# Optimization experiments

Hardware: AMD Instinct MI355X
Metric: run time of the kernel (lower is better)

The kernel has to match this reference:

```python
import jax, jax.numpy as jnp
import numpy as np


def setup_inputs() -> dict:
    key = jax.random.key(0)
    k1, k2, k3 = jax.random.split(key, 3)
    N1, N2, P, D = 4, 8, 1024, 128  # P = PH*PW = 32*32 (512px / 16 patch)
    feats = jax.random.normal(k1, (N1, P, D), dtype=jnp.float32)
    nfeats = jax.random.normal(k2, (N2, P, D), dtype=jnp.float32)
    background_masks = jax.random.uniform(k3, (N1, P), dtype=jnp.float32)
    return {"feats": feats, "nfeats": nfeats, "background_masks": background_masks,
            "PH": 32, "PW": 32, "H": 512, "W": 512}


def reference(feats, nfeats, background_masks, PH, PW, H, W):
    # L2-normalize patch embeddings (as in `f / f.norm(dim=-1, keepdim=True)`)
    f = feats / jnp.linalg.norm(feats, axis=-1, keepdims=True)    # [N1,P,D]
    g = nfeats / jnp.linalg.norm(nfeats, axis=-1, keepdims=True)  # [N2,Q,D]
    # Euclidean cdist of unit vectors: d^2 = 2 - 2*dot (clamped at 0)
    dot = jnp.einsum('npd,mqd->nmpq', f, g)                        # [N1,N2,P,Q]
    dist = jnp.sqrt(jnp.maximum(2.0 - 2.0 * dot, 0.0)) / 2.0      # cdist/2, permuted
    # min over normal patches Q -> per-query-patch nearest-neighbor distance
    scores_patch = dist.min(axis=-1)                               # [N1,N2,P]
    scores_patch = scores_patch * background_masks[:, None, :]
    # image score: max over query patches, mean over normal images
    scores = scores_patch.max(axis=-1).mean(axis=-1)               # [N1]
    # pixel map: mean over normal images, reshape to patch grid, bilinear upsample
    sp = scores_patch.mean(axis=1).reshape(-1, PH, PW)             # [N1,PH,PW]
    scores_pixel = jax.image.resize(sp, (sp.shape[0], H, W), method='bilinear')
    return scores, scores_pixel
```

## Files before the change

### kernel.cpp

```cpp
#include <hip/hip_runtime.h>

typedef __attribute__((ext_vector_type(8))) short short8;
typedef __attribute__((ext_vector_type(4))) float f32x4;
typedef __attribute__((ext_vector_type(4))) unsigned int u32x4;

static __device__ inline unsigned short f2bf(float x) {
    unsigned int u = __float_as_uint(x);
    u = (u + 0x7FFFu + ((u >> 16) & 1u)) >> 16;
    return (unsigned short)u;
}

__global__ __launch_bounds__(256) void knorm(const float* __restrict__ feats,
                                             const float* __restrict__ nfeats,
                                             unsigned short* __restrict__ fb,
                                             unsigned short* __restrict__ gb) {
    int row = blockIdx.x * 4 + (threadIdx.x >> 6);
    int lane = threadIdx.x & 63;
    const float* src;
    unsigned short* dst;
    if (row < 4096) { src = feats + row * 128;           dst = fb + row * 128; }
    else            { src = nfeats + (row - 4096) * 128; dst = gb + (row - 4096) * 128; }
    float2 v = ((const float2*)src)[lane];
    float ss = v.x * v.x + v.y * v.y;
    #pragma unroll
    for (int d = 32; d; d >>= 1) ss += __shfl_xor(ss, d);
    float inv = 1.0f / sqrtf(ss);
    ushort2 o;
    o.x = f2bf(v.x * inv);
    o.y = f2bf(v.y * inv);
    ((ushort2*)dst)[lane] = o;
}

__global__ __launch_bounds__(512, 2) void kscore(const unsigned short* __restrict__ fb,
                                                 const unsigned short* __restrict__ gb,
                                                 float* __restrict__ sp_part) {
    __shared__ char gtile[2][8192];
    const int tid = threadIdx.x;
    const int lane = tid & 63;
    const int wave = tid >> 6;
    const int wp = wave >> 1, wqt = wave & 1;
    const int l15 = lane & 15, lhi = lane >> 4;
    const int m = blockIdx.x;
    const int ptile = blockIdx.y >> 1, qh = blockIdx.y & 1;
    const int rowbase = ptile * 256 + wp * 64;

    const unsigned short* gBase = gb + ((size_t)m * 1024 + qh * 512) * 128;

    const int sr = tid >> 4, sc = tid & 15;
    const unsigned short* gsrc = gBase + (size_t)sr * 128 + sc * 8;
    const int wofs = (sr * 256 + sc * 16) ^ ((sr & 7) << 4);

    short8 a[4][4];
    #pragma unroll
    for (int pg = 0; pg < 4; pg++) {
        const unsigned short* arow = fb + (size_t)(rowbase + pg * 16 + l15) * 128;
        #pragma unroll
        for (int kk = 0; kk < 4; kk++)
            a[pg][kk] = *(const short8*)(arow + kk * 32 + lhi * 8);
    }

    f32x4 mx[4];
    #pragma unroll
    for (int pg = 0; pg < 4; pg++)
        #pragma unroll
        for (int i = 0; i < 4; i++) mx[pg][i] = -1e30f;

    u32x4 st0 = *(const u32x4*)(gsrc);
    *(u32x4*)(gtile[0] + wofs) = st0;
    u32x4 stn = *(const u32x4*)(gsrc + 32 * 128);
    asm volatile("s_waitcnt lgkmcnt(0)" ::: "memory");
    __builtin_amdgcn_s_barrier();

    #pragma unroll
    for (int t = 0; t < 16; t++) {
        __builtin_amdgcn_sched_barrier(0);
        u32x4 stnn;
        if (t < 14) stnn = *(const u32x4*)(gsrc + (size_t)(t + 2) * 32 * 128);
        if (t < 15) *(u32x4*)(gtile[(t + 1) & 1] + wofs) = stn;
        const char* tp = gtile[t & 1];
        const int r = wqt * 16 + l15;
        const int rowoff = r * 256;
        const int swz = (r & 7) << 4;
        f32x4 acc[4];
        #pragma unroll
        for (int pg = 0; pg < 4; pg++)
            #pragma unroll
            for (int i = 0; i < 4; i++) acc[pg][i] = 0.f;
        #pragma unroll
        for (int kk = 0; kk < 4; kk++) {
            short8 b = *(const short8*)(tp + ((rowoff + kk * 64 + lhi * 16) ^ swz));
            #pragma unroll
            for (int pg = 0; pg < 4; pg++)
                acc[pg] = __builtin_amdgcn_mfma_f32_16x16x32_bf16(a[pg][kk], b, acc[pg], 0, 0, 0);
        }
        #pragma unroll
        for (int pg = 0; pg < 4; pg++)
            #pragma unroll
            for (int i = 0; i < 4; i++) mx[pg][i] = fmaxf(mx[pg][i], acc[pg][i]);
        if (t < 14) stn = stnn;
        asm volatile("s_waitcnt lgkmcnt(0)" ::: "memory");
        __builtin_amdgcn_s_barrier();
    }

    #pragma unroll
    for (int pg = 0; pg < 4; pg++)
        #pragma unroll
        for (int i = 0; i < 4; i++) {
            float v = mx[pg][i];
            v = fmaxf(v, __shfl_xor(v, 1));
            v = fmaxf(v, __shfl_xor(v, 2));
            v = fmaxf(v, __shfl_xor(v, 4));
            v = fmaxf(v, __shfl_xor(v, 8));
            mx[pg][i] = v;
        }
    if (l15 == 0) {
        const int slot = qh * 2 + wqt;
        #pragma unroll
        for (int pg = 0; pg < 4; pg++)
            #pragma unroll
            for (int i = 0; i < 4; i++) {
                int row = rowbase + pg * 16 + lhi * 4 + i;
                int n = row >> 10, p = row & 1023;
                sp_part[((size_t)(n * 8 + m) * 4 + slot) * 1024 + p] = mx[pg][i];
            }
    }
}

__global__ __launch_bounds__(256) void kfinal(const float* __restrict__ sp_part,
                                              const float* __restrict__ mask,
                                              float* __restrict__ out) {
    const int n = blockIdx.y;
    const int bx = blockIdx.x;
    const int t = threadIdx.x;
    float* pix = out + 4;

    if (bx == 64) {
        __shared__ float smax[4];
        float acc = 0.f;
        for (int m = 0; m < 8; m++) {
            const float* base = sp_part + (size_t)(n * 8 + m) * 4 * 1024;
            float lm = -1e30f;
            #pragma unroll
            for (int i = 0; i < 4; i++) {
                int p = i * 256 + t;
                float dot = fmaxf(fmaxf(base[p], base[1024 + p]),
                                  fmaxf(base[2048 + p], base[3072 + p]));
                float d = sqrtf(fmaxf(2.0f - 2.0f * dot, 0.0f)) * 0.5f * mask[n * 1024 + p];
                lm = fmaxf(lm, d);
            }
            #pragma unroll
            for (int d = 32; d; d >>= 1) lm = fmaxf(lm, __shfl_xor(lm, d));
            if ((t & 63) == 0) smax[t >> 6] = lm;
            __syncthreads();
            if (t == 0) acc += fmaxf(fmaxf(smax[0], smax[1]), fmaxf(smax[2], smax[3]));
            __syncthreads();
        }
        if (t == 0) out[n] = acc * 0.125f;
        return;
    }

    __shared__ float sp_row[2][32];
    const int band = bx * 8;
    const int pr_lo = (int)floorf((band + 0.5f) * 0.0625f - 0.5f);
    const int row0 = min(max(pr_lo, 0), 31);
    const int row1 = min(max(pr_lo + 1, 0), 31);
    {
        int v = t >> 2, sub = t & 3;
        int vr = v >> 5, vc = v & 31;
        int p = (vr ? row1 : row0) * 32 + vc;
        float sum = 0.f;
        #pragma unroll
        for (int mi = 0; mi < 2; mi++) {
            int m = sub * 2 + mi;
            const float* base = sp_part + (size_t)(n * 8 + m) * 4 * 1024 + p;
            float dot = fmaxf(fmaxf(base[0], base[1024]),
                              fmaxf(base[2048], base[3072]));
            sum += sqrtf(fmaxf(2.0f - 2.0f * dot, 0.0f)) * 0.5f;
        }
        sum *= mask[n * 1024 + p];
        sum += __shfl_xor(sum, 1);
        sum += __shfl_xor(sum, 2);
        if (sub == 0) sp_row[vr][vc] = sum * 0.125f;
    }
    __syncthreads();
    #pragma unroll
    for (int i = 0; i < 16; i++) {
        int idx = i * 256 + t;
        int yl = idx >> 9, x = idx & 511;
        int y = band + yl;
        float fy = (y + 0.5f) * 0.0625f - 0.5f;
        float ty = fy - (float)pr_lo;
        float fx = (x + 0.5f) * 0.0625f - 0.5f;
        float xf = floorf(fx);
        float tx = fx - xf;
        int x0 = (int)xf;
        int x0c = min(max(x0, 0), 31), x1c = min(max(x0 + 1, 0), 31);
        float v00 = sp_row[0][x0c], v01 = sp_row[0][x1c];
        float v10 = sp_row[1][x0c], v11 = sp_row[1][x1c];
        float v0 = v00 + tx * (v01 - v00);
        float v1 = v10 + tx * (v11 - v10);
        pix[(size_t)n * 262144 + (size_t)y * 512 + x] = v0 + ty * (v1 - v0);
    }
}

extern "C" void kernel_launch(void* const* d_in, const int* in_sizes, int n_in,
                              void* d_out, int out_size, void* d_ws, size_t ws_size,
                              hipStream_t stream) {
    const float* feats = (const float*)d_in[0];
    const float* nfeats = (const float*)d_in[1];
    const float* mask = (const float*)d_in[2];
    float* out = (float*)d_out;

    unsigned short* fb = (unsigned short*)d_ws;
    unsigned short* gb = fb + 4096 * 128;
    float* sp_part = (float*)((char*)d_ws + 3u * 1024u * 1024u);

    knorm<<<3072, 256, 0, stream>>>(feats, nfeats, fb, gb);
    kscore<<<dim3(8, 32), 512, 0, stream>>>(fb, gb, sp_part);
    kfinal<<<dim3(65, 4), 256, 0, stream>>>(sp_part, mask, out);
}
```

Baseline: 31.05 us.

## Split kscore into 256-thread blocks covering quarter Q ranges, each wave doing both q-tiles

```diff
diff --git a/kernel.cpp b/kernel.cpp
--- a/kernel.cpp
+++ b/kernel.cpp
@@ -31,24 +31,26 @@
     ((ushort2*)dst)[lane] = o;
 }
 
-__global__ __launch_bounds__(512, 2) void kscore(const unsigned short* __restrict__ fb,
+__global__ __launch_bounds__(256, 2) void kscore(const unsigned short* __restrict__ fb,
                                                  const unsigned short* __restrict__ gb,
                                                  float* __restrict__ sp_part) {
     __shared__ char gtile[2][8192];
     const int tid = threadIdx.x;
     const int lane = tid & 63;
     const int wave = tid >> 6;
-    const int wp = wave >> 1, wqt = wave & 1;
     const int l15 = lane & 15, lhi = lane >> 4;
     const int m = blockIdx.x;
-    const int ptile = blockIdx.y >> 1, qh = blockIdx.y & 1;
-    const int rowbase = ptile * 256 + wp * 64;
-
-    const unsigned short* gBase = gb + ((size_t)m * 1024 + qh * 512) * 128;
-
-    const int sr = tid >> 4, sc = tid & 15;
-    const unsigned short* gsrc = gBase + (size_t)sr * 128 + sc * 8;
-    const int wofs = (sr * 256 + sc * 16) ^ ((sr & 7) << 4);
+    const int ptile = blockIdx.y >> 2, qq = blockIdx.y & 3;
+    const int rowbase = ptile * 256 + wave * 64;
+
+    const unsigned short* gBase = gb + ((size_t)m * 1024 + qq * 256) * 128;
+
+    const int r0 = tid >> 4, s0 = tid & 15;
+    const int r1 = r0 + 16;
+    const unsigned short* gsrc0 = gBase + (size_t)r0 * 128 + s0 * 8;
+    const unsigned short* gsrc1 = gBase + (size_t)r1 * 128 + s0 * 8;
+    const int wofs0 = (r0 * 256 + s0 * 16) ^ ((r0 & 7) << 4);
+    const int wofs1 = (r1 * 256 + s0 * 16) ^ ((r1 & 7) << 4);
 
     short8 a[4][4];
     #pragma unroll
@@ -65,39 +67,51 @@
         #pragma unroll
         for (int i = 0; i < 4; i++) mx[pg][i] = -1e30f;
 
-    u32x4 st0 = *(const u32x4*)(gsrc);
-    *(u32x4*)(gtile[0] + wofs) = st0;
-    u32x4 stn = *(const u32x4*)(gsrc + 32 * 128);
+    u32x4 t0a = *(const u32x4*)(gsrc0);
+    u32x4 t0b = *(const u32x4*)(gsrc1);
+    *(u32x4*)(gtile[0] + wofs0) = t0a;
+    *(u32x4*)(gtile[0] + wofs1) = t0b;
+    u32x4 stna = *(const u32x4*)(gsrc0 + 32 * 128);
+    u32x4 stnb = *(const u32x4*)(gsrc1 + 32 * 128);
     asm volatile("s_waitcnt lgkmcnt(0)" ::: "memory");
     __builtin_amdgcn_s_barrier();
 
     #pragma unroll
-    for (int t = 0; t < 16; t++) {
+    for (int t = 0; t < 8; t++) {
         __builtin_amdgcn_sched_barrier(0);
-        u32x4 stnn;
-        if (t < 14) stnn = *(const u32x4*)(gsrc + (size_t)(t + 2) * 32 * 128);
-        if (t < 15) *(u32x4*)(gtile[(t + 1) & 1] + wofs) = stn;
+        u32x4 s2a, s2b;
+        if (t < 6) {
+            s2a = *(const u32x4*)(gsrc0 + (size_t)(t + 2) * 32 * 128);
+            s2b = *(const u32x4*)(gsrc1 + (size_t)(t + 2) * 32 * 128);
+        }
+        if (t < 7) {
+            *(u32x4*)(gtile[(t + 1) & 1] + wofs0) = stna;
+            *(u32x4*)(gtile[(t + 1) & 1] + wofs1) = stnb;
+        }
         const char* tp = gtile[t & 1];
-        const int r = wqt * 16 + l15;
-        const int rowoff = r * 256;
-        const int swz = (r & 7) << 4;
-        f32x4 acc[4];
-        #pragma unroll
-        for (int pg = 0; pg < 4; pg++)
-            #pragma unroll
-            for (int i = 0; i < 4; i++) acc[pg][i] = 0.f;
-        #pragma unroll
-        for (int kk = 0; kk < 4; kk++) {
-            short8 b = *(const short8*)(tp + ((rowoff + kk * 64 + lhi * 16) ^ swz));
+        #pragma unroll
+        for (int qt = 0; qt < 2; qt++) {
+            const int r = qt * 16 + l15;
+            const int rowoff = r * 256;
+            const int swz = (r & 7) << 4;
+            f32x4 acc[4];
             #pragma unroll
             for (int pg = 0; pg < 4; pg++)
-                acc[pg] = __builtin_amdgcn_mfma_f32_16x16x32_bf16(a[pg][kk], b, acc[pg], 0, 0, 0);
-        }
-        #pragma unroll
-        for (int pg = 0; pg < 4; pg++)
-            #pragma unroll
-            for (int i = 0; i < 4; i++) mx[pg][i] = fmaxf(mx[pg][i], acc[pg][i]);
-        if (t < 14) stn = stnn;
+                #pragma unroll
+                for (int i = 0; i < 4; i++) acc[pg][i] = 0.f;
+            #pragma unroll
+            for (int kk = 0; kk < 4; kk++) {
+                short8 b = *(const short8*)(tp + ((rowoff + kk * 64 + lhi * 16) ^ swz));
+                #pragma unroll
+                for (int pg = 0; pg < 4; pg++)
+                    acc[pg] = __builtin_amdgcn_mfma_f32_16x16x32_bf16(a[pg][kk], b, acc[pg], 0, 0, 0);
+            }
+            #pragma unroll
+            for (int pg = 0; pg < 4; pg++)
+                #pragma unroll
+                for (int i = 0; i < 4; i++) mx[pg][i] = fmaxf(mx[pg][i], acc[pg][i]);
+        }
+        if (t < 6) { stna = s2a; stnb = s2b; }
         asm volatile("s_waitcnt lgkmcnt(0)" ::: "memory");
         __builtin_amdgcn_s_barrier();
     }
@@ -114,14 +128,13 @@
             mx[pg][i] = v;
         }
     if (l15 == 0) {
-        const int slot = qh * 2 + wqt;
         #pragma unroll
         for (int pg = 0; pg < 4; pg++)
             #pragma unroll
             for (int i = 0; i < 4; i++) {
                 int row = rowbase + pg * 16 + lhi * 4 + i;
                 int n = row >> 10, p = row & 1023;
-                sp_part[((size_t)(n * 8 + m) * 4 + slot) * 1024 + p] = mx[pg][i];
+                sp_part[((size_t)(n * 8 + m) * 4 + qq) * 1024 + p] = mx[pg][i];
             }
     }
 }
@@ -216,6 +229,6 @@
     float* sp_part = (float*)((char*)d_ws + 3u * 1024u * 1024u);
 
     knorm<<<3072, 256, 0, stream>>>(feats, nfeats, fb, gb);
-    kscore<<<dim3(8, 32), 512, 0, stream>>>(fb, gb, sp_part);
+    kscore<<<dim3(8, 64), 256, 0, stream>>>(fb, gb, sp_part);
     kfinal<<<dim3(65, 4), 256, 0, stream>>>(sp_part, mask, out);
 }
```

After: 30.09 us. -3.1%, faster.
